# Optimization experiments

Measured on AMD Instinct MI355X. Metric: run time of the kernel, lower is better.

The kernel has to match this reference:

```python
import jax, jax.numpy as jnp
import numpy as np

VOCAB = 128000
B, S = 1024, 8192
LR_PLUS = 0.01
TAU = 5.0
DECAY = 0.99
W_MIN, W_MAX = 0.0, 1.0
TRACE_DECAY = float(np.exp(-1.0 / TAU))


def setup_inputs() -> dict:
    key = jax.random.key(0)
    k1, k2, k3 = jax.random.split(key, 3)
    token_ids = jax.random.randint(k1, (B, S), 0, VOCAB, dtype=jnp.int64 if jax.config.jax_enable_x64 else jnp.int32)
    # Bernoulli-like spikes in {0,1}: threshold a uniform draw (still float input)
    spikes = (jax.random.uniform(k2, (B, S), dtype=jnp.float32) < 0.3).astype(jnp.float32)
    token_weights = jnp.full((VOCAB,), 0.5, dtype=jnp.float32)
    del k3
    return {"token_ids": token_ids, "spikes": spikes, "token_weights": token_weights}


def _traces(spikes):
    # curr_trace[t] = curr_trace[t-1] * TRACE_DECAY + spikes[:, t]
    td = jnp.asarray(TRACE_DECAY, spikes.dtype)

    def step(carry, s_t):
        carry = carry * td + s_t
        return carry, carry

    init = jnp.zeros((spikes.shape[0],), spikes.dtype)
    _, tr = jax.lax.scan(step, init, spikes.T)  # [S, B]
    return tr.T  # [B, S]


def reference(token_ids, spikes, token_weights):
    traces = _traces(spikes)                      # [B, S]
    updates = LR_PLUS * traces * spikes           # [B, S]
    grad_accum = jnp.zeros_like(token_weights).at[token_ids.reshape(-1)].add(
        updates.reshape(-1)
    )
    new_w = jnp.clip((token_weights + grad_accum) * DECAY, W_MIN, W_MAX)
    return new_w
```

## Files before the change

kernel.cpp:

```cpp
#include <hip/hip_runtime.h>


#define VOCAB_N 128000
#define B_ROWS  1024
#define S_LEN   8192
#define NRANGE  8
#define VR      16000
#define VR2     (VR / 2)
#define G2      32
#define CAP     512
#define ROWS_PER_BIN (B_ROWS / G2)

constexpr float TRACE_DECAY = 0.8187307530779818586699355f;
constexpr float A16 = 0.040762203978366211696f;
constexpr float LR_PLUS = 0.01f;
constexpr float W_DECAY = 0.99f;

__device__ __forceinline__ unsigned f32_to_bf16_rtne(float x) {
    unsigned b = __float_as_uint(x);
    b += 0x7FFFu + ((b >> 16) & 1u);
    return b >> 16;
}

__global__ __launch_bounds__(512) void stdp_scan_pack(
    const int* __restrict__ token_ids,
    const float* __restrict__ spikes,
    unsigned* __restrict__ counts,
    unsigned* __restrict__ pairs)
{
    const int row  = blockIdx.x;
    const int tid  = threadIdx.x;
    const int lane = tid & 63;
    const int wid  = tid >> 6;
    const long base = (long)row * S_LEN + (long)tid * 16;

    float s[16];
    int   tok[16];
    {
        const float4* sp4 = reinterpret_cast<const float4*>(spikes + base);
        const int4*   tk4 = reinterpret_cast<const int4*>(token_ids + base);
        float4 a0 = sp4[0], a1 = sp4[1], a2 = sp4[2], a3 = sp4[3];
        int4   b0 = tk4[0], b1 = tk4[1], b2 = tk4[2], b3 = tk4[3];
        s[0]=a0.x; s[1]=a0.y; s[2]=a0.z; s[3]=a0.w;
        s[4]=a1.x; s[5]=a1.y; s[6]=a1.z; s[7]=a1.w;
        s[8]=a2.x; s[9]=a2.y; s[10]=a2.z; s[11]=a2.w;
        s[12]=a3.x; s[13]=a3.y; s[14]=a3.z; s[15]=a3.w;
        tok[0]=b0.x; tok[1]=b0.y; tok[2]=b0.z; tok[3]=b0.w;
        tok[4]=b1.x; tok[5]=b1.y; tok[6]=b1.z; tok[7]=b1.w;
        tok[8]=b2.x; tok[9]=b2.y; tok[10]=b2.z; tok[11]=b2.w;
        tok[12]=b3.x; tok[13]=b3.y; tok[14]=b3.z; tok[15]=b3.w;
    }

    float L = 0.f;
    #pragma unroll
    for (int j = 0; j < 16; ++j) L = fmaf(L, TRACE_DECAY, s[j]);

    unsigned long long rpack = 0ull, cnt_lo = 0ull, cnt_hi = 0ull;
    #pragma unroll
    for (int j = 0; j < 16; ++j) {
        int r = tok[j] / VR;
        rpack |= (unsigned long long)r << (4 * j);
        if (s[j] != 0.f) {
            if (r < 4) cnt_lo += 1ull << (r << 4);
            else       cnt_hi += 1ull << ((r - 4) << 4);
        }
    }

    float A = A16, Bv = L;
    unsigned long long ilo = cnt_lo, ihi = cnt_hi;
    #pragma unroll
    for (int o = 1; o < 64; o <<= 1) {
        float Ao = __shfl_up(A, o);
        float Bo = __shfl_up(Bv, o);
        unsigned long long ulo = __shfl_up(ilo, o);
        unsigned long long uhi = __shfl_up(ihi, o);
        if (lane >= o) { Bv = fmaf(A, Bo, Bv); A = A * Ao; ilo += ulo; ihi += uhi; }
    }

    __shared__ float wAf[8], wBf[8];
    __shared__ unsigned long long wlo[8], whi[8];
    __shared__ unsigned bcnt[NRANGE];
    __shared__ unsigned stage[NRANGE][CAP];
    if (lane == 63) { wAf[wid] = A; wBf[wid] = Bv; wlo[wid] = ilo; whi[wid] = ihi; }
    __syncthreads();

    float carry = 0.f;
    unsigned long long blo = 0ull, bhi = 0ull;
    #pragma unroll
    for (int w = 0; w < 7; ++w)
        if (w < wid) {
            carry = fmaf(wAf[w], carry, wBf[w]);
            blo += wlo[w]; bhi += whi[w];
        }

    float Ae = __shfl_up(A, 1), Be = __shfl_up(Bv, 1);
    if (lane == 0) { Ae = 1.f; Be = 0.f; }
    float trace = fmaf(Ae, carry, Be);

    unsigned long long offlo = (ilo - cnt_lo) + blo;
    unsigned long long offhi = (ihi - cnt_hi) + bhi;

    if (tid < NRANGE) {
        unsigned long long t = 0ull;
        unsigned c;
        if (tid < 4) {
            #pragma unroll
            for (int w = 0; w < 8; ++w) t += wlo[w];
            c = (unsigned)((t >> (tid * 16)) & 0xFFFFull);
        } else {
            #pragma unroll
            for (int w = 0; w < 8; ++w) t += whi[w];
            c = (unsigned)((t >> ((tid - 4) * 16)) & 0xFFFFull);
        }
        counts[row * NRANGE + tid] = c;
        bcnt[tid] = c > CAP ? CAP : c;
    }

    {
        float tr = trace;
        #pragma unroll
        for (int j = 0; j < 16; ++j) {
            tr = fmaf(tr, TRACE_DECAY, s[j]);
            if (s[j] != 0.f) {
                float upd = LR_PLUS * tr;
                unsigned pk = (f32_to_bf16_rtne(upd) << 17) | (unsigned)tok[j];
                int r = (int)((rpack >> (4 * j)) & 0xFull);
                unsigned slot;
                if (r < 4) {
                    int sh = r << 4;
                    slot = (unsigned)((offlo >> sh) & 0xFFFFull);
                    offlo += 1ull << sh;
                } else {
                    int sh = (r - 4) << 4;
                    slot = (unsigned)((offhi >> sh) & 0xFFFFull);
                    offhi += 1ull << sh;
                }
                if (slot < CAP) stage[r][slot] = pk;
            }
        }
    }
    __syncthreads();

    #pragma unroll
    for (int k = 0; k < (NRANGE * CAP) / 512; ++k) {
        int idx = k * 512 + tid;
        int r = idx >> 9;
        int i = idx & (CAP - 1);
        if ((unsigned)i < bcnt[r])
            pairs[((size_t)r * B_ROWS + row) * CAP + i] = stage[r][i];
    }
}

__global__ __launch_bounds__(512) void stdp_bin(
    const unsigned* __restrict__ counts,
    const unsigned* __restrict__ pairs,
    unsigned* __restrict__ part)
{
    __shared__ float bins[VR];
    __shared__ unsigned ccache[ROWS_PER_BIN];
    const int r = blockIdx.x >> 5;
    const int g = blockIdx.x & 31;
    const int row0 = g * ROWS_PER_BIN;

    float4* b4 = reinterpret_cast<float4*>(bins);
    for (int i = threadIdx.x; i < VR / 4; i += 512)
        b4[i] = make_float4(0.f, 0.f, 0.f, 0.f);
    if (threadIdx.x < ROWS_PER_BIN) {
        unsigned c = counts[(row0 + threadIdx.x) * NRANGE + r];
        ccache[threadIdx.x] = c > CAP ? CAP : c;
    }
    __syncthreads();

    const unsigned* bp = pairs + ((size_t)r * B_ROWS + row0) * CAP;
    const int rbase = r * VR;
    #pragma unroll 4
    for (int idx = threadIdx.x; idx < ROWS_PER_BIN * CAP; idx += 512) {
        int rr = idx >> 9;
        int i  = idx & (CAP - 1);
        if ((unsigned)i < ccache[rr]) {
            unsigned p = bp[idx];
            int t = (int)(p & 0x1FFFFu) - rbase;
            float v = __uint_as_float((p >> 17) << 16);
            atomicAdd(&bins[t], v);
        }
    }
    __syncthreads();

    unsigned* o = part + ((size_t)(r * G2 + g)) * VR2;
    for (int i = threadIdx.x; i < VR2; i += 512) {
        unsigned lo = f32_to_bf16_rtne(bins[2 * i]);
        unsigned hi = f32_to_bf16_rtne(bins[2 * i + 1]);
        o[i] = lo | (hi << 16);
    }
}

__global__ __launch_bounds__(256) void stdp_reduce(
    const float* __restrict__ token_weights,
    const unsigned* __restrict__ part,
    float* __restrict__ out)
{
    int c = blockIdx.x * 256 + threadIdx.x;
    if (c >= VOCAB_N / 2) return;
    int r = c / VR2;
    int l = c - r * VR2;
    const unsigned* p = part + (size_t)r * G2 * VR2 + l;
    float a0 = 0.f, a1 = 0.f;
    #pragma unroll
    for (int g = 0; g < G2; ++g) {
        unsigned u = p[(size_t)g * VR2];
        a0 += __uint_as_float(u << 16);
        a1 += __uint_as_float(u & 0xFFFF0000u);
    }
    float2 w = reinterpret_cast<const float2*>(token_weights)[c];
    float2 o;
    o.x = fminf(fmaxf((w.x + a0) * W_DECAY, 0.f), 1.f);
    o.y = fminf(fmaxf((w.y + a1) * W_DECAY, 0.f), 1.f);
    reinterpret_cast<float2*>(out)[c] = o;
}

__global__ __launch_bounds__(512) void stdp_scan_scatter(
    const int* __restrict__ token_ids,
    const float* __restrict__ spikes,
    float* __restrict__ grad)
{
    const int row  = blockIdx.x;
    const int tid  = threadIdx.x;
    const int lane = tid & 63;
    const int wid  = tid >> 6;
    const long base = (long)row * S_LEN + (long)tid * 16;

    float s[16]; int tok[16];
    {
        const float4* sp4 = reinterpret_cast<const float4*>(spikes + base);
        const int4*   tk4 = reinterpret_cast<const int4*>(token_ids + base);
        float4 a0 = sp4[0], a1 = sp4[1], a2 = sp4[2], a3 = sp4[3];
        int4   b0 = tk4[0], b1 = tk4[1], b2 = tk4[2], b3 = tk4[3];
        s[0]=a0.x; s[1]=a0.y; s[2]=a0.z; s[3]=a0.w;
        s[4]=a1.x; s[5]=a1.y; s[6]=a1.z; s[7]=a1.w;
        s[8]=a2.x; s[9]=a2.y; s[10]=a2.z; s[11]=a2.w;
        s[12]=a3.x; s[13]=a3.y; s[14]=a3.z; s[15]=a3.w;
        tok[0]=b0.x; tok[1]=b0.y; tok[2]=b0.z; tok[3]=b0.w;
        tok[4]=b1.x; tok[5]=b1.y; tok[6]=b1.z; tok[7]=b1.w;
        tok[8]=b2.x; tok[9]=b2.y; tok[10]=b2.z; tok[11]=b2.w;
        tok[12]=b3.x; tok[13]=b3.y; tok[14]=b3.z; tok[15]=b3.w;
    }

    float L = 0.f;
    #pragma unroll
    for (int j = 0; j < 16; ++j) L = fmaf(L, TRACE_DECAY, s[j]);
    float A = A16, Bv = L;
    #pragma unroll
    for (int o = 1; o < 64; o <<= 1) {
        float Ao = __shfl_up(A, o);
        float Bo = __shfl_up(Bv, o);
        if (lane >= o) { Bv = fmaf(A, Bo, Bv); A = A * Ao; }
    }
    __shared__ float wA[8], wB[8];
    if (lane == 63) { wA[wid] = A; wB[wid] = Bv; }
    __syncthreads();
    float carry = 0.f;
    #pragma unroll
    for (int w = 0; w < 7; ++w)
        if (w < wid) carry = fmaf(wA[w], carry, wB[w]);
    float Ae = __shfl_up(A, 1), Be = __shfl_up(Bv, 1);
    if (lane == 0) { Ae = 1.f; Be = 0.f; }
    float trace = fmaf(Ae, carry, Be);

    #pragma unroll
    for (int j = 0; j < 16; ++j) {
        trace = fmaf(trace, TRACE_DECAY, s[j]);
        if (s[j] != 0.f) atomicAdd(&grad[tok[j]], LR_PLUS * trace);
    }
}

__global__ __launch_bounds__(256) void stdp_finalize(
    const float* __restrict__ token_weights,
    float* __restrict__ out, int n)
{
    int v = blockIdx.x * 256 + threadIdx.x;
    if (v < n) {
        float g = out[v];
        float w = (token_weights[v] + g) * W_DECAY;
        out[v] = fminf(fmaxf(w, 0.f), 1.f);
    }
}

extern "C" void kernel_launch(void* const* d_in, const int* in_sizes, int n_in,
                              void* d_out, int out_size, void* d_ws, size_t ws_size,
                              hipStream_t stream) {
    const int*   token_ids = (const int*)d_in[0];
    const float* spikes    = (const float*)d_in[1];
    const float* tw        = (const float*)d_in[2];
    float* out = (float*)d_out;

    const size_t counts_elems = (size_t)B_ROWS * NRANGE;
    const size_t pairs_elems  = (size_t)NRANGE * B_ROWS * CAP;
    const size_t part_elems   = (size_t)NRANGE * G2 * VR2;
    const size_t need = (counts_elems + pairs_elems + part_elems) * 4;

    if (ws_size >= need) {
        unsigned* counts = (unsigned*)d_ws;
        unsigned* pairs  = counts + counts_elems;
        unsigned* part   = pairs + pairs_elems;

        stdp_scan_pack<<<B_ROWS, 512, 0, stream>>>(token_ids, spikes,
                                                   counts, pairs);
        stdp_bin<<<NRANGE * G2, 512, 0, stream>>>(counts, pairs, part);
        stdp_reduce<<<(VOCAB_N / 2 + 255) / 256, 256, 0, stream>>>(tw, part, out);
    } else {
        hipMemsetAsync(out, 0, (size_t)out_size * sizeof(float), stream);
        stdp_scan_scatter<<<B_ROWS, 512, 0, stream>>>(token_ids, spikes, out);
        stdp_finalize<<<(out_size + 255) / 256, 256, 0, stream>>>(tw, out,
                                                                  out_size);
    }
}
```

Before: 46.36 us.

## Double bin-kernel row groups and prefetch pairs as uint4 before smem clear

Doubles the number of row groups per vocab range in the binning kernel, so each block handles 16 rows instead of 32 and the grid is twice as large. Each thread now issues four 16-byte vector loads of packed pairs up front, before zeroing the shared-memory bins, so global load latency overlaps the clear and sync. The atomic accumulation loop is unrolled over the preloaded registers. In exchange, twice as many partial bf16 histograms are written and later reduced, which raises memory traffic in the reduce stage.

```diff
diff --git a/kernel.cpp b/kernel.cpp
--- a/kernel.cpp
+++ b/kernel.cpp
@@ -7,7 +7,7 @@
 #define NRANGE  8
 #define VR      16000
 #define VR2     (VR / 2)
-#define G2      32
+#define G2      64
 #define CAP     512
 #define ROWS_PER_BIN (B_ROWS / G2)
 
@@ -158,9 +158,16 @@
 {
     __shared__ float bins[VR];
     __shared__ unsigned ccache[ROWS_PER_BIN];
-    const int r = blockIdx.x >> 5;
-    const int g = blockIdx.x & 31;
+    const int r = blockIdx.x >> 6;
+    const int g = blockIdx.x & (G2 - 1);
     const int row0 = g * ROWS_PER_BIN;
+
+    const uint4* bp4 = reinterpret_cast<const uint4*>(
+        pairs + ((size_t)r * B_ROWS + row0) * CAP);
+    const uint4 q0 = bp4[threadIdx.x];
+    const uint4 q1 = bp4[threadIdx.x + 512];
+    const uint4 q2 = bp4[threadIdx.x + 1024];
+    const uint4 q3 = bp4[threadIdx.x + 1536];
 
     float4* b4 = reinterpret_cast<float4*>(bins);
     for (int i = threadIdx.x; i < VR / 4; i += 512)
@@ -171,19 +178,29 @@
     }
     __syncthreads();
 
-    const unsigned* bp = pairs + ((size_t)r * B_ROWS + row0) * CAP;
     const int rbase = r * VR;
-    #pragma unroll 4
-    for (int idx = threadIdx.x; idx < ROWS_PER_BIN * CAP; idx += 512) {
-        int rr = idx >> 9;
-        int i  = idx & (CAP - 1);
-        if ((unsigned)i < ccache[rr]) {
-            unsigned p = bp[idx];
-            int t = (int)(p & 0x1FFFFu) - rbase;
-            float v = __uint_as_float((p >> 17) << 16);
-            atomicAdd(&bins[t], v);
-        }
-    }
+    #define BIN_Q(q, idx4)                                                   \
+    {                                                                        \
+        int rr = (idx4) >> 7;                                  \
+        unsigned i0 = ((idx4) & 127) << 2;                   \
+        unsigned c = ccache[rr];                                             \
+        unsigned pv[4] = {(q).x, (q).y, (q).z, (q).w};                       \
+        _Pragma("unroll")                                                    \
+        for (int sub = 0; sub < 4; ++sub) {                                  \
+            if (i0 + sub < c) {                                              \
+                unsigned p = pv[sub];                                        \
+                int t = (int)(p & 0x1FFFFu) - rbase;                         \
+                float v = __uint_as_float((p >> 17) << 16);                  \
+                atomicAdd(&bins[t], v);                                      \
+            }                                                                \
+        }                                                                    \
+    }
+
+    BIN_Q(q0, (int)threadIdx.x);
+    BIN_Q(q1, (int)threadIdx.x + 512);
+    BIN_Q(q2, (int)threadIdx.x + 1024);
+    BIN_Q(q3, (int)threadIdx.x + 1536);
+    #undef BIN_Q
     __syncthreads();
 
     unsigned* o = part + ((size_t)(r * G2 + g)) * VR2;
```

After: 48.02 us. +3.6%, slower.
